# Performance work log

Measured on AMD Instinct MI355X. Metric: run time of the kernel, lower is better.

The kernel has to match this reference:

```python
import jax, jax.numpy as jnp
import numpy as np

MOMENTUM = 0.99
EPS = 1e-5


def setup_inputs() -> dict:
    key = jax.random.key(0)
    k1, k2, k3, k4 = jax.random.split(key, 4)
    x = jax.random.normal(k1, (16, 256, 64, 64), dtype=jnp.float32)
    embed = jax.random.normal(k2, (2048, 256), dtype=jnp.float32)
    cluster_size = jax.random.uniform(k3, (2048,), dtype=jnp.float32)
    embed_avg = jax.random.normal(k4, (256, 2048), dtype=jnp.float32)
    return {"x": x, "embed": embed, "cluster_size": cluster_size, "embed_avg": embed_avg}


def reference(x, embed, cluster_size, embed_avg):
    # x: (b, c, h, w) with c == emb_dim; embed: (D, c)
    b, c, h, w = x.shape
    D = embed.shape[0]
    # flatten exactly as the torch code: transpose(1,-1) then reshape(-1, c)
    flat = jnp.swapaxes(x, 1, 3).reshape(-1, c)  # (N, c), N = b*w*h
    # L2 kNN with k=1, expressed as argmax of 2*q.k - |k|^2 - |q|^2 (as in _torch_knn)
    scores = (2.0 * (flat @ embed.T)
              - jnp.sum(embed * embed, axis=1)[None, :]
              - jnp.sum(flat * flat, axis=1, keepdims=True))  # (N, D)
    ids_flat = jnp.argmax(scores, axis=1)  # (N,)
    ids = ids_flat.reshape(b, h, w)
    # lookup + transpose(1,-1), mirroring the original op sequence
    quantized = jnp.swapaxes(embed[ids], 1, 3)  # (b, c, w, h) == (b, c, h, w) since h == w
    commit_loss = jnp.mean((x - quantized) ** 2)
    # EMA statistics (training branch). one-hot matmul expressed as segment sums (same math).
    onehot_sum = jax.ops.segment_sum(jnp.ones_like(ids_flat, dtype=flat.dtype), ids_flat,
                                     num_segments=D)  # (D,)
    embed_sum = jax.ops.segment_sum(flat, ids_flat, num_segments=D).T  # (c, D) == flat.T @ onehot
    new_cluster_size = MOMENTUM * cluster_size + (1.0 - MOMENTUM) * onehot_sum
    new_embed_avg = MOMENTUM * embed_avg + (1.0 - MOMENTUM) * embed_sum
    n = jnp.sum(new_cluster_size)
    cs_smoothed = n * (new_cluster_size + EPS) / (n + D * EPS)
    new_embed = new_embed_avg.T / cs_smoothed[:, None]  # (D, c)
    return quantized, commit_loss, ids, new_embed, new_cluster_size, new_embed_avg
```

## Files before the change

kernel.cpp:

```cpp
#include <hip/hip_runtime.h>

#define D_CODES 2048
#define C_DIM   256
#define MOM     0.99f
#define ONE_M   0.01f
#define EPSI    1e-5f
#define TAU     0.16f
#define RCAP    16384
#define SBCAP   2304

#define Q_OFF    0
#define LOSS_OFF 16777216
#define IDS_OFF  16777217
#define NE_OFF   16842753
#define NCS_OFF  17367041
#define NEA_OFF  17369089

#define WS_ICNT    0
#define WS_CNTF    2048
#define WS_OFFS    4096
#define WS_CURS    6144
#define WS_SUMX2   10240
#define WS_NTOT    11264
#define WS_RCNT    11268
#define WS_NSB     11269
#define WS_NORMS   11272
#define WS_RLIST   13320
#define WS_ESUM    29704
#define WS_E2      553992
#define WS_KEYH    816136
#define WS_M2H     1078280
#define WS_PLIST   1209352
#define WS_SBCODE  1274888
#define WS_SBSTART 1277192
#define WS_SBINFO  1279496
#define WS_LOSSP   1281800

typedef _Float16 half8 __attribute__((ext_vector_type(8)));
typedef __attribute__((ext_vector_type(4))) float f32x4;
typedef unsigned long long u64;

__device__ __forceinline__ f32x4 MFH(half8 a, half8 b, f32x4 c) {
    return __builtin_amdgcn_mfma_f32_16x16x32_f16(a, b, c, 0, 0, 0);
}
__device__ __forceinline__ unsigned enc_f(float v) {
    unsigned u = __float_as_uint(v);
    return (u & 0x80000000u) ? ~u : (u | 0x80000000u);
}
__device__ __forceinline__ float dec_f(unsigned u) {
    return (u & 0x80000000u) ? __uint_as_float(u & 0x7FFFFFFFu)
                             : __uint_as_float(~u);
}

__global__ __launch_bounds__(256) void k_init(
    const float* __restrict__ embed, float* __restrict__ e2f,
    float* __restrict__ norms, float* __restrict__ esum,
    int* __restrict__ icnt, float* __restrict__ lossp,
    unsigned* __restrict__ rcnt, float* __restrict__ etg)
{
    const int b = blockIdx.x, t = threadIdx.x;
    esum[(size_t)b * 256 + t] = 0.f;
    if (b < 64) {
        __shared__ float nrm[32];
        if (t < 32) nrm[t] = 0.f;
        __syncthreads();
        char* e2 = (char*)e2f;
        const int s = b;
        #pragma unroll
        for (int it = 0; it < 4; ++it) {
            int u = it * 256 + t;
            int r = u >> 9, kc = (u >> 6) & 7, l = u & 63;
            int code = s * 32 + r * 16 + (l & 15);
            int ch0  = kc * 32 + ((l >> 4) << 3);
            const float* src = embed + (size_t)code * C_DIM + ch0;
            float4 v0 = *(const float4*)src;
            float4 v1 = *(const float4*)(src + 4);
            float vv[8] = {v0.x, v0.y, v0.z, v0.w, v1.x, v1.y, v1.z, v1.w};
            half8 hh;
            float p = 0.f;
            #pragma unroll
            for (int j = 0; j < 8; ++j) { hh[j] = (_Float16)vv[j]; p += vv[j] * vv[j]; }
            atomicAdd(&nrm[r * 16 + (l & 15)], p);
            char* dst = e2 + (size_t)s * 16384 + (size_t)((r * 8 + kc) * 64 + l) * 16;
            *(half8*)dst = hh;
        }
        __syncthreads();
        if (t < 32) norms[s * 32 + t] = nrm[t];
    } else if (b < 72) {
        icnt[(b - 64) * 256 + t] = 0;
    } else if (b < 81) {
        int j = (b - 72) * 256 + t;
        if (j < SBCAP) lossp[j] = 0.f;
    } else if (b == 81) {
        if (t == 0) *rcnt = 0u;
    } else if (b >= 128 && b < 384) {
        int code0 = (b - 128) * 8;
        #pragma unroll
        for (int j = 0; j < 8; ++j) {
            float v = embed[(size_t)(code0 + j) * C_DIM + t];
            etg[(size_t)t * D_CODES + code0 + j] = v;
        }
    }
}

__device__ __forceinline__ void stage_copy(const char* __restrict__ g, char* lds_base,
                                           int w, int l) {
    #pragma unroll
    for (int i = 0; i < 4; ++i) {
        int off = w * 4096 + i * 1024;
        __builtin_amdgcn_global_load_lds(
            (const __attribute__((address_space(1))) void*)(g + off + l * 16),
            (__attribute__((address_space(3))) void*)(lds_base + off),
            16, 0, 0);
    }
}

__global__ __launch_bounds__(256, 2) void k_main(
    const float* __restrict__ x, const float* __restrict__ e2f,
    const float* __restrict__ norms, float* __restrict__ xt,
    float* __restrict__ sumx2p, u64* __restrict__ keyh,
    float* __restrict__ m2h)
{
    __shared__ char smem[33280];
    __shared__ float wred[4];
    const int t  = threadIdx.x;
    const int l  = t & 63;
    const int w  = __builtin_amdgcn_readfirstlane(t >> 6);
    const int blk = blockIdx.x;
    const int h  = blk & 1;
    const int q  = (blk >> 1) & 31;
    const int bi = blk >> 6;
    const char* e2 = (const char*)e2f + (size_t)h * 32 * 16384;

    half8 bx[2][8];
    float sx2 = 0.f;
    {
        float* xs = (float*)smem;
        const int hiq = w >> 1;
        const int wib = (w & 1) * 32;
        for (int c = 0; c < 4; ++c) {
            __syncthreads();
            #pragma unroll
            for (int k = 0; k < 8; ++k) {
                int u = k * 256 + t;
                int wi0 = (u & 15) * 4;
                int hq  = (u >> 4) & 1;
                int chl = u >> 5;
                float4 v = *(const float4*)(x + ((size_t)(bi * C_DIM + c * 64 + chl)) * 4096
                                              + (2 * q + hq) * 64 + wi0);
                if (h == 0) sx2 += v.x * v.x + v.y * v.y + v.z * v.z + v.w * v.w;
                int pb = (hq * 64 + wi0) * 65 + chl;
                xs[pb] = v.x; xs[pb + 65] = v.y; xs[pb + 130] = v.z; xs[pb + 195] = v.w;
            }
            __syncthreads();
            if (h == 1) {
                int plo = t >> 4;
                int cc4 = (t & 15) * 4;
                #pragma unroll
                for (int p8 = 0; p8 < 8; ++p8) {
                    int pl = p8 * 16 + plo;
                    const float* sp = &xs[pl * 65 + cc4];
                    float4 f = {sp[0], sp[1], sp[2], sp[3]};
                    int hq = pl >> 6, wi = pl & 63;
                    size_t n = (size_t)bi * 4096 + (size_t)wi * 64 + (2 * q + hq);
                    *(float4*)(xt + n * C_DIM + c * 64 + cc4) = f;
                }
            }
            #pragma unroll
            for (int kcl = 0; kcl < 2; ++kcl) {
                #pragma unroll
                for (int nt = 0; nt < 2; ++nt) {
                    int pl = hiq * 64 + wib + nt * 16 + (l & 15);
                    const float* src = &xs[pl * 65 + kcl * 32 + ((l >> 4) << 3)];
                    half8 hh;
                    #pragma unroll
                    for (int j = 0; j < 8; ++j) hh[j] = (_Float16)src[j];
                    bx[nt][c * 2 + kcl] = hh;
                }
            }
        }
        __syncthreads();
    }
    if (h == 0) {
        #pragma unroll
        for (int o = 32; o; o >>= 1) sx2 += __shfl_down(sx2, o);
        if (l == 0) wred[w] = sx2;
    }

    float m1[2] = {-3.4e38f, -3.4e38f}, m2[2] = {-3.4e38f, -3.4e38f};
    int   i1[2] = {0, 0};

    stage_copy(e2, smem, w, l);
    __syncthreads();

    for (int s = 0; s < 32; ++s) {
        char* cur = smem + (s & 1) * 16384;
        if (s < 31)
            stage_copy(e2 + (size_t)(s + 1) * 16384, smem + ((s + 1) & 1) * 16384, w, l);

        #pragma unroll
        for (int r = 0; r < 2; ++r) {
            f32x4 z = {0.f, 0.f, 0.f, 0.f};
            f32x4 aA0 = z, aA1 = z;
            #pragma unroll
            for (int kc = 0; kc < 8; ++kc) {
                half8 ah = *(const half8*)(cur + ((r * 8 + kc) * 64 + l) * 16);
                aA0 = MFH(ah, bx[0][kc], aA0);
                aA1 = MFH(ah, bx[1][kc], aA1);
            }
            int c0 = h * 1024 + s * 32 + r * 16 + ((l >> 4) << 2);
            float4 nrm = *(const float4*)(norms + c0);
            float nr[4] = {nrm.x, nrm.y, nrm.z, nrm.w};
            #pragma unroll
            for (int reg = 0; reg < 4; ++reg) {
                float s0 = 2.f * aA0[reg] - nr[reg];
                float s1 = 2.f * aA1[reg] - nr[reg];
                int code = c0 + reg;
                if (s0 > m1[0]) { m2[0] = m1[0]; m1[0] = s0; i1[0] = code; }
                else            { m2[0] = fmaxf(m2[0], s0); }
                if (s1 > m1[1]) { m2[1] = m1[1]; m1[1] = s1; i1[1] = code; }
                else            { m2[1] = fmaxf(m2[1], s1); }
            }
        }
        __syncthreads();
    }

    #pragma unroll
    for (int nt = 0; nt < 2; ++nt) {
        float a1 = m1[nt], a2 = m2[nt];
        int   ai = i1[nt];
        #pragma unroll
        for (int off = 16; off <= 32; off <<= 1) {
            float o1 = __shfl_xor(a1, off);
            int   oi = __shfl_xor(ai, off);
            float o2 = __shfl_xor(a2, off);
            if (o1 > a1)       { a2 = fmaxf(a1, o2); a1 = o1; ai = oi; }
            else if (o1 == a1) { if (oi < ai) ai = oi; a2 = a1; }
            else               { a2 = fmaxf(a2, o1); }
        }
        if (l < 16) {
            int wi = (w & 1) * 32 + nt * 16 + l;
            int hi_ = 2 * q + (w >> 1);
            int n = (bi << 12) + (wi << 6) + hi_;
            keyh[((size_t)h << 16) + n] = ((u64)enc_f(a1) << 32) | (unsigned)(~ai);
            m2h[(h << 16) + n] = a2;
        }
    }
    if (h == 0) {
        __syncthreads();
        if (t == 0) sumx2p[bi * 32 + q] = wred[0] + wred[1] + wred[2] + wred[3];
    }
}

__global__ __launch_bounds__(256) void k_merge(
    const u64* __restrict__ keyh, const float* __restrict__ m2h,
    float* __restrict__ out, int* __restrict__ icnt,
    unsigned* __restrict__ rcnt, int* __restrict__ rlist)
{
    int n = blockIdx.x * 256 + threadIdx.x;
    u64 kA = keyh[n], kB = keyh[65536 + n];
    float m2A = m2h[n], m2B = m2h[65536 + n];
    bool wA = kA >= kB;
    u64 kW = wA ? kA : kB, kL = wA ? kB : kA;
    float m2w = wA ? m2A : m2B;
    float sW = dec_f((unsigned)(kW >> 32));
    float sL = dec_f((unsigned)(kL >> 32));
    int code = (int)(~(unsigned)kW);
    out[IDS_OFF + n] = (float)code;
    atomicAdd(&icnt[code], 1);
    float gap = sW - fmaxf(m2w, sL);
    if (gap < TAU) {
        unsigned j = atomicAdd(rcnt, 1u);
        if (j < RCAP) rlist[j] = n;
    }
}

__global__ __launch_bounds__(256) void k_rescue(
    const float* __restrict__ xt, const float* __restrict__ etg,
    const float* __restrict__ norms, const unsigned* __restrict__ rcnt,
    const int* __restrict__ rlist, float* __restrict__ out,
    int* __restrict__ icnt)
{
    __shared__ float xs[8][257];
    __shared__ int nn[8];
    __shared__ u64 rk[4][8];
    const int t = threadIdx.x;
    const int l = t & 63;
    const int w = t >> 6;
    int nf = (int)min(*rcnt, (unsigned)RCAP);
    int nch = (nf + 7) >> 3;
    for (int chunk = blockIdx.x; chunk < nch; chunk += gridDim.x) {
        __syncthreads();
        if (t < 8) {
            int idx = chunk * 8 + t;
            nn[t] = rlist[idx < nf ? idx : (nf - 1)];
        }
        __syncthreads();
        #pragma unroll
        for (int p = 0; p < 8; ++p)
            xs[p][t] = xt[(size_t)nn[p] * C_DIM + t];
        __syncthreads();
        u64 bk[8];
        #pragma unroll
        for (int p = 0; p < 8; ++p) bk[p] = 0ull;
        #pragma unroll
        for (int rep = 0; rep < 2; ++rep) {
            const int d0 = rep * 1024 + t * 4;
            f32x4 acc[8];
            #pragma unroll
            for (int p = 0; p < 8; ++p) acc[p] = (f32x4){0.f, 0.f, 0.f, 0.f};
            for (int c = 0; c < C_DIM; ++c) {
                float4 e4 = *(const float4*)(etg + (size_t)c * D_CODES + d0);
                f32x4 ev = {e4.x, e4.y, e4.z, e4.w};
                #pragma unroll
                for (int p = 0; p < 8; ++p)
                    acc[p] += xs[p][c] * ev;
            }
            float4 nr = *(const float4*)(norms + d0);
            float nrr[4] = {nr.x, nr.y, nr.z, nr.w};
            #pragma unroll
            for (int p = 0; p < 8; ++p) {
                #pragma unroll
                for (int j = 0; j < 4; ++j) {
                    float sc = 2.f * acc[p][j] - nrr[j];
                    u64 key = ((u64)enc_f(sc) << 32) | (unsigned)(~(d0 + j));
                    if (key > bk[p]) bk[p] = key;
                }
            }
        }
        #pragma unroll
        for (int p = 0; p < 8; ++p) {
            u64 k0 = bk[p];
            #pragma unroll
            for (int o = 32; o; o >>= 1) {
                u64 ok = __shfl_down(k0, o);
                if (ok > k0) k0 = ok;
            }
            if (l == 0) rk[w][p] = k0;
        }
        __syncthreads();
        if (t < 8 && chunk * 8 + t < nf) {
            u64 k0 = rk[0][t];
            if (rk[1][t] > k0) k0 = rk[1][t];
            if (rk[2][t] > k0) k0 = rk[2][t];
            if (rk[3][t] > k0) k0 = rk[3][t];
            int n = nn[t];
            int newid = (int)(~(unsigned)k0);
            int old = (int)out[IDS_OFF + n];
            if (newid != old) {
                out[IDS_OFF + n] = (float)newid;
                atomicAdd(&icnt[old], -1);
                atomicAdd(&icnt[newid], 1);
            }
        }
    }
}

__global__ __launch_bounds__(256) void k_prefix(const int* __restrict__ icnt,
                                                const float* __restrict__ cs_in,
                                                int* __restrict__ offs,
                                                int* __restrict__ curs,
                                                float* __restrict__ cntf,
                                                int* __restrict__ sbcode,
                                                int* __restrict__ sbstart,
                                                int* __restrict__ sbinfo,
                                                int* __restrict__ nsbtot,
                                                float* __restrict__ ntot) {
    __shared__ int ps[256];
    __shared__ float fs[256];
    const int t = threadIdx.x;
    int c[8], o8[8];
    int s = 0;
    #pragma unroll
    for (int j = 0; j < 8; ++j) c[j] = icnt[t * 8 + j];
    #pragma unroll
    for (int j = 0; j < 8; ++j) { int tmp = c[j]; c[j] = s; s += tmp; }
    ps[t] = s;
    __syncthreads();
    for (int off = 1; off < 256; off <<= 1) {
        int v = (t >= off) ? ps[t - off] : 0;
        __syncthreads();
        ps[t] += v;
        __syncthreads();
    }
    int base = ps[t] - s;
    #pragma unroll
    for (int j = 0; j < 8; ++j) {
        int o = base + c[j];
        o8[j] = o;
        offs[t * 8 + j] = o;
        curs[t * 8 + j] = o;
        cntf[t * 8 + j] = (float)(icnt[t * 8 + j]);
    }
    int s2 = 0;
    int nb[8];
    #pragma unroll
    for (int j = 0; j < 8; ++j) {
        int cnt = icnt[t * 8 + j];
        nb[j] = (cnt + 255) >> 8;
        s2 += nb[j];
    }
    __syncthreads();
    ps[t] = s2;
    __syncthreads();
    for (int off = 1; off < 256; off <<= 1) {
        int v = (t >= off) ? ps[t - off] : 0;
        __syncthreads();
        ps[t] += v;
        __syncthreads();
    }
    int pos = ps[t] - s2;
    #pragma unroll
    for (int j = 0; j < 8; ++j) {
        int code = t * 8 + j;
        int cnt = icnt[code];
        int n = nb[j];
        for (int k = 0; k < n; ++k) {
            sbcode[pos]  = code;
            sbstart[pos] = o8[j] + k * 256;
            int len = cnt - k * 256; if (len > 256) len = 256;
            sbinfo[pos]  = len | ((n > 1) ? (1 << 16) : 0);
            ++pos;
        }
    }
    if (t == 255) *nsbtot = ps[255];
    float s3 = 0.f;
    #pragma unroll
    for (int j = 0; j < 8; ++j) s3 += cs_in[t * 8 + j];
    fs[t] = s3;
    __syncthreads();
    for (int o = 128; o; o >>= 1) { if (t < o) fs[t] += fs[t + o]; __syncthreads(); }
    if (t == 0) *ntot = MOM * fs[0] + ONE_M * 65536.0f;
}

__global__ __launch_bounds__(256) void k_scatter(const float* __restrict__ out,
                                                 int* __restrict__ curs,
                                                 int* __restrict__ plist) {
    int n = blockIdx.x * 256 + threadIdx.x;
    int id = (int)out[IDS_OFF + n];
    int pos = atomicAdd(&curs[id], 1);
    plist[pos] = n;
}

__global__ __launch_bounds__(256) void k_esum(
    const float* __restrict__ xt, const float* __restrict__ embed,
    const float* __restrict__ norms, const int* __restrict__ sbcode,
    const int* __restrict__ sbstart, const int* __restrict__ sbinfo,
    const int* __restrict__ plist, const int* __restrict__ nsbtot,
    float* __restrict__ esum, float* __restrict__ lossp)
{
    __shared__ int   ns[256];
    __shared__ float red[256];
    const int t = threadIdx.x;
    const int total = *nsbtot;
    for (int sb = blockIdx.x; sb < total; sb += gridDim.x) {
        const int d     = sbcode[sb];
        const int start = sbstart[sb];
        const int info  = sbinfo[sb];
        const int len   = info & 0xFFFF;
        const bool multi = (info >> 16) != 0;
        __syncthreads();
        if (t < len) ns[t] = plist[start + t];
        __syncthreads();
        float acc = 0.f;
        #pragma unroll 8
        for (int i = 0; i < len; ++i)
            acc += xt[(size_t)ns[i] * C_DIM + t];
        if (multi) atomicAdd(&esum[(size_t)t * D_CODES + d], acc);
        else       esum[(size_t)t * D_CODES + d] = acc;
        red[t] = acc * embed[(size_t)d * C_DIM + t];
        __syncthreads();
        for (int o = 128; o; o >>= 1) {
            if (t < o) red[t] += red[t + o];
            __syncthreads();
        }
        if (t == 0) lossp[sb] = 2.f * red[0] - (float)len * norms[d];
    }
}

__global__ __launch_bounds__(256) void k_quant(
    const float* __restrict__ embed, float* __restrict__ out)
{
    __shared__ int   ids_s[64];
    __shared__ float es[32][257];
    const int t  = threadIdx.x;
    const int bi = blockIdx.x >> 6;
    const int hi = blockIdx.x & 63;
    const int wl = t & 31;
    const int cg = t >> 5;
    if (t < 64) ids_s[t] = (int)out[IDS_OFF + ((size_t)bi << 12) + (t << 6) + hi];
    __syncthreads();
    #pragma unroll
    for (int pass = 0; pass < 2; ++pass) {
        #pragma unroll 8
        for (int p = 0; p < 32; ++p) {
            es[p][t] = embed[(size_t)ids_s[pass * 32 + p] * C_DIM + t];
        }
        __syncthreads();
        #pragma unroll 8
        for (int k = 0; k < 32; ++k) {
            int ch = k * 8 + cg;
            out[Q_OFF + ((size_t)(bi * C_DIM + ch)) * 4096 + hi * 64 + pass * 32 + wl]
                = es[wl][ch];
        }
        __syncthreads();
    }
}

__global__ __launch_bounds__(256) void k_final(
    const float* __restrict__ cs_in, const float* __restrict__ cntf,
    const float* __restrict__ embed_avg, const float* __restrict__ esum,
    const float* __restrict__ ntotp, const float* __restrict__ lossp,
    const float* __restrict__ sumx2p, float* __restrict__ out)
{
    const int b = blockIdx.x;
    const int t = threadIdx.x;
    if (b < 2048) {
        int ch = b >> 3;
        int d  = ((b & 7) << 8) + t;
        float ntot = *ntotp;
        float ncs  = MOM * cs_in[d] + ONE_M * cntf[d];
        if (b < 8) out[NCS_OFF + d] = ncs;
        float csm  = ntot * (ncs + EPSI) / (ntot + (float)D_CODES * EPSI);
        size_t i = (size_t)ch * D_CODES + d;
        float nea = MOM * embed_avg[i] + ONE_M * esum[i];
        out[NEA_OFF + i] = nea;
        out[NE_OFF + (size_t)d * C_DIM + ch] = nea / csm;
    } else {
        __shared__ float sm[256];
        float s1 = 0.f;
        for (int i = t; i < 512; i += 256) s1 += sumx2p[i];
        float s2 = 0.f;
        for (int i = t; i < SBCAP; i += 256) s2 += lossp[i];
        sm[t] = s1 - s2;
        __syncthreads();
        for (int o = 128; o; o >>= 1) { if (t < o) sm[t] += sm[t + o]; __syncthreads(); }
        if (t == 0) out[LOSS_OFF] = sm[0] / 16777216.f;
    }
}

extern "C" void kernel_launch(void* const* d_in, const int* in_sizes, int n_in,
                              void* d_out, int out_size, void* d_ws, size_t ws_size,
                              hipStream_t stream) {
    const float* x     = (const float*)d_in[0];
    const float* embed = (const float*)d_in[1];
    const float* cs    = (const float*)d_in[2];
    const float* ea    = (const float*)d_in[3];
    float* out = (float*)d_out;
    float* ws  = (float*)d_ws;
    int*      icnt    = (int*)(ws + WS_ICNT);
    float*    cntf    = ws + WS_CNTF;
    int*      offs    = (int*)(ws + WS_OFFS);
    int*      curs    = (int*)(ws + WS_CURS);
    float*    sumx2p  = ws + WS_SUMX2;
    float*    ntot    = ws + WS_NTOT;
    unsigned* rcnt    = (unsigned*)(ws + WS_RCNT);
    int*      nsbtot  = (int*)(ws + WS_NSB);
    float*    norms   = ws + WS_NORMS;
    int*      rlist   = (int*)(ws + WS_RLIST);
    float*    esum    = ws + WS_ESUM;
    float*    e2      = ws + WS_E2;
    u64*      keyh    = (u64*)(ws + WS_KEYH);
    float*    m2h     = ws + WS_M2H;
    int*      plist   = (int*)(ws + WS_PLIST);
    int*      sbcode  = (int*)(ws + WS_SBCODE);
    int*      sbstart = (int*)(ws + WS_SBSTART);
    int*      sbinfo  = (int*)(ws + WS_SBINFO);
    float*    lossp   = ws + WS_LOSSP;
    float*    xt      = out + Q_OFF;
    float*    etg     = out + NEA_OFF;

    k_init<<<2048, 256, 0, stream>>>(embed, e2, norms, esum, icnt, lossp, rcnt, etg);
    k_main<<<1024, 256, 0, stream>>>(x, e2, norms, xt, sumx2p, keyh, m2h);
    k_merge<<<256, 256, 0, stream>>>(keyh, m2h, out, icnt, rcnt, rlist);
    k_rescue<<<512, 256, 0, stream>>>(xt, etg, norms, rcnt, rlist, out, icnt);
    k_prefix<<<1, 256, 0, stream>>>(icnt, cs, offs, curs, cntf, sbcode, sbstart,
                                    sbinfo, nsbtot, ntot);
    k_scatter<<<256, 256, 0, stream>>>(out, curs, plist);
    k_esum<<<SBCAP, 256, 0, stream>>>(xt, embed, norms, sbcode, sbstart, sbinfo,
                                      plist, nsbtot, esum, lossp);
    k_quant<<<1024, 256, 0, stream>>>(embed, out);
    k_final<<<2049, 256, 0, stream>>>(cs, cntf, ea, esum, ntot, lossp, sumx2p, out);
}
```

Before: 293.2 us.

## Double pixels per k_main block to reuse each codebook A-fragment across four N-tiles

Each k_main block now handles 256 pixels (four rows of h) instead of 128, so each wave holds four half8 B-fragment sets and issues four MFMAs per codebook A-fragment read from LDS. The grid halves to 512 blocks, which halves the total codebook staging traffic from e2 and the LDS reads per MFMA. The x staging tile is rearranged to a channel-major layout with padding 258 and float2 stores, and it is processed in eight 32-channel chunks. The cost is more registers per thread (bx grows to 32 half8 values plus more accumulators), which may reduce occupancy under launch_bounds(256,2), and fewer blocks in the grid.

```diff
diff --git a/kernel.cpp b/kernel.cpp
--- a/kernel.cpp
+++ b/kernel.cpp
@@ -121,62 +121,62 @@
     float* __restrict__ sumx2p, u64* __restrict__ keyh,
     float* __restrict__ m2h)
 {
-    __shared__ char smem[33280];
+    __shared__ char smem[33024];
     __shared__ float wred[4];
     const int t  = threadIdx.x;
     const int l  = t & 63;
     const int w  = __builtin_amdgcn_readfirstlane(t >> 6);
     const int blk = blockIdx.x;
     const int h  = blk & 1;
-    const int q  = (blk >> 1) & 31;
-    const int bi = blk >> 6;
+    const int q  = (blk >> 1) & 15;
+    const int bi = blk >> 5;
     const char* e2 = (const char*)e2f + (size_t)h * 32 * 16384;
 
-    half8 bx[2][8];
+    half8 bx[4][8];
     float sx2 = 0.f;
     {
         float* xs = (float*)smem;
-        const int hiq = w >> 1;
-        const int wib = (w & 1) * 32;
-        for (int c = 0; c < 4; ++c) {
+        #pragma unroll
+        for (int c = 0; c < 8; ++c) {
             __syncthreads();
             #pragma unroll
             for (int k = 0; k < 8; ++k) {
                 int u = k * 256 + t;
-                int wi0 = (u & 15) * 4;
-                int hq  = (u >> 4) & 1;
-                int chl = u >> 5;
-                float4 v = *(const float4*)(x + ((size_t)(bi * C_DIM + c * 64 + chl)) * 4096
-                                              + (2 * q + hq) * 64 + wi0);
+                int wi0 = (u & 15) << 2;
+                int hq  = (u >> 4) & 3;
+                int chl = u >> 6;
+                float4 v = *(const float4*)(x + ((size_t)(bi * C_DIM + c * 32 + chl)) * 4096
+                                              + (4 * q + hq) * 64 + wi0);
                 if (h == 0) sx2 += v.x * v.x + v.y * v.y + v.z * v.z + v.w * v.w;
-                int pb = (hq * 64 + wi0) * 65 + chl;
-                xs[pb] = v.x; xs[pb + 65] = v.y; xs[pb + 130] = v.z; xs[pb + 195] = v.w;
+                int pb = chl * 258 + hq * 64 + wi0;
+                *(float2*)&xs[pb]     = make_float2(v.x, v.y);
+                *(float2*)&xs[pb + 2] = make_float2(v.z, v.w);
             }
             __syncthreads();
             if (h == 1) {
-                int plo = t >> 4;
-                int cc4 = (t & 15) * 4;
+                int ch4 = (t & 7) * 4;
+                int pxo = t >> 3;
                 #pragma unroll
-                for (int p8 = 0; p8 < 8; ++p8) {
-                    int pl = p8 * 16 + plo;
-                    const float* sp = &xs[pl * 65 + cc4];
-                    float4 f = {sp[0], sp[1], sp[2], sp[3]};
-                    int hq = pl >> 6, wi = pl & 63;
-                    size_t n = (size_t)bi * 4096 + (size_t)wi * 64 + (2 * q + hq);
-                    *(float4*)(xt + n * C_DIM + c * 64 + cc4) = f;
+                for (int it = 0; it < 8; ++it) {
+                    int px = it * 32 + pxo;
+                    float v0 = xs[(ch4 + 0) * 258 + px];
+                    float v1 = xs[(ch4 + 1) * 258 + px];
+                    float v2 = xs[(ch4 + 2) * 258 + px];
+                    float v3 = xs[(ch4 + 3) * 258 + px];
+                    int hq = px >> 6, wi = px & 63;
+                    size_t n = (size_t)bi * 4096 + (size_t)wi * 64 + (4 * q + hq);
+                    *(float4*)(xt + n * C_DIM + c * 32 + ch4) = make_float4(v0, v1, v2, v3);
                 }
             }
             #pragma unroll
-            for (int kcl = 0; kcl < 2; ++kcl) {
+            for (int nt = 0; nt < 4; ++nt) {
+                int px = w * 64 + nt * 16 + (l & 15);
+                const int cb = (l >> 4) << 3;
+                half8 hh;
                 #pragma unroll
-                for (int nt = 0; nt < 2; ++nt) {
-                    int pl = hiq * 64 + wib + nt * 16 + (l & 15);
-                    const float* src = &xs[pl * 65 + kcl * 32 + ((l >> 4) << 3)];
-                    half8 hh;
-                    #pragma unroll
-                    for (int j = 0; j < 8; ++j) hh[j] = (_Float16)src[j];
-                    bx[nt][c * 2 + kcl] = hh;
-                }
+                for (int j = 0; j < 8; ++j)
+                    hh[j] = (_Float16)xs[(cb + j) * 258 + px];
+                bx[nt][c] = hh;
             }
         }
         __syncthreads();
@@ -187,8 +187,9 @@
         if (l == 0) wred[w] = sx2;
     }
 
-    float m1[2] = {-3.4e38f, -3.4e38f}, m2[2] = {-3.4e38f, -3.4e38f};
-    int   i1[2] = {0, 0};
+    float m1[4] = {-3.4e38f, -3.4e38f, -3.4e38f, -3.4e38f};
+    float m2[4] = {-3.4e38f, -3.4e38f, -3.4e38f, -3.4e38f};
+    int   i1[4] = {0, 0, 0, 0};
 
     stage_copy(e2, smem, w, l);
     __syncthreads();
@@ -201,32 +202,33 @@
         #pragma unroll
         for (int r = 0; r < 2; ++r) {
             f32x4 z = {0.f, 0.f, 0.f, 0.f};
-            f32x4 aA0 = z, aA1 = z;
+            f32x4 aA[4] = {z, z, z, z};
             #pragma unroll
             for (int kc = 0; kc < 8; ++kc) {
                 half8 ah = *(const half8*)(cur + ((r * 8 + kc) * 64 + l) * 16);
-                aA0 = MFH(ah, bx[0][kc], aA0);
-                aA1 = MFH(ah, bx[1][kc], aA1);
+                #pragma unroll
+                for (int nt = 0; nt < 4; ++nt)
+                    aA[nt] = MFH(ah, bx[nt][kc], aA[nt]);
             }
             int c0 = h * 1024 + s * 32 + r * 16 + ((l >> 4) << 2);
             float4 nrm = *(const float4*)(norms + c0);
             float nr[4] = {nrm.x, nrm.y, nrm.z, nrm.w};
             #pragma unroll
-            for (int reg = 0; reg < 4; ++reg) {
-                float s0 = 2.f * aA0[reg] - nr[reg];
-                float s1 = 2.f * aA1[reg] - nr[reg];
-                int code = c0 + reg;
-                if (s0 > m1[0]) { m2[0] = m1[0]; m1[0] = s0; i1[0] = code; }
-                else            { m2[0] = fmaxf(m2[0], s0); }
-                if (s1 > m1[1]) { m2[1] = m1[1]; m1[1] = s1; i1[1] = code; }
-                else            { m2[1] = fmaxf(m2[1], s1); }
-            }
-        }
-        __syncthreads();
-    }
-
-    #pragma unroll
-    for (int nt = 0; nt < 2; ++nt) {
+            for (int nt = 0; nt < 4; ++nt) {
+                #pragma unroll
+                for (int reg = 0; reg < 4; ++reg) {
+                    float sc = 2.f * aA[nt][reg] - nr[reg];
+                    int code = c0 + reg;
+                    if (sc > m1[nt]) { m2[nt] = m1[nt]; m1[nt] = sc; i1[nt] = code; }
+                    else             { m2[nt] = fmaxf(m2[nt], sc); }
+                }
+            }
+        }
+        __syncthreads();
+    }
+
+    #pragma unroll
+    for (int nt = 0; nt < 4; ++nt) {
         float a1 = m1[nt], a2 = m2[nt];
         int   ai = i1[nt];
         #pragma unroll
@@ -239,8 +241,8 @@
             else               { a2 = fmaxf(a2, o1); }
         }
         if (l < 16) {
-            int wi = (w & 1) * 32 + nt * 16 + l;
-            int hi_ = 2 * q + (w >> 1);
+            int wi = nt * 16 + l;
+            int hi_ = 4 * q + w;
             int n = (bi << 12) + (wi << 6) + hi_;
             keyh[((size_t)h << 16) + n] = ((u64)enc_f(a1) << 32) | (unsigned)(~ai);
             m2h[(h << 16) + n] = a2;
@@ -248,7 +250,7 @@
     }
     if (h == 0) {
         __syncthreads();
-        if (t == 0) sumx2p[bi * 32 + q] = wred[0] + wred[1] + wred[2] + wred[3];
+        if (t == 0) sumx2p[bi * 16 + q] = wred[0] + wred[1] + wred[2] + wred[3];
     }
 }
 
@@ -528,8 +530,7 @@
         out[NE_OFF + (size_t)d * C_DIM + ch] = nea / csm;
     } else {
         __shared__ float sm[256];
-        float s1 = 0.f;
-        for (int i = t; i < 512; i += 256) s1 += sumx2p[i];
+        float s1 = sumx2p[t];
         float s2 = 0.f;
         for (int i = t; i < SBCAP; i += 256) s2 += lossp[i];
         sm[t] = s1 - s2;
@@ -571,7 +572,7 @@
     float*    etg     = out + NEA_OFF;
 
     k_init<<<2048, 256, 0, stream>>>(embed, e2, norms, esum, icnt, lossp, rcnt, etg);
-    k_main<<<1024, 256, 0, stream>>>(x, e2, norms, xt, sumx2p, keyh, m2h);
+    k_main<<<512, 256, 0, stream>>>(x, e2, norms, xt, sumx2p, keyh, m2h);
     k_merge<<<256, 256, 0, stream>>>(keyh, m2h, out, icnt, rcnt, rlist);
     k_rescue<<<512, 256, 0, stream>>>(xt, etg, norms, rcnt, rlist, out, icnt);
     k_prefix<<<1, 256, 0, stream>>>(icnt, cs, offs, curs, cntf, sbcode, sbstart,
```

Result: slower. 396.4 us (+35.2%).
